# Performance work log

Hardware: AMD Instinct MI355X
Metric: run time of the kernel (lower is better)

The kernel has to match this reference:

```python
import jax, jax.numpy as jnp
import numpy as np
from jax import lax

# mamba-130m-style config
B, L = 2, 1024          # batch, seq_len
D = 768                 # hidden_size
E = 1536                # intermediate (expand=2)
N = 16                  # ssm state size
R = 48                  # time_step_rank = ceil(D/16)
K = 4                   # conv kernel
NL = 4                  # num layers
NC = 5                  # num classes
EPS = 1e-5


def setup_inputs() -> dict:
    key = jax.random.key(0)
    ks = jax.random.split(key, 10)
    s = 0.02
    return {
        "x": jax.random.normal(ks[0], (B, L, 12), dtype=jnp.float32),
        "proj_w": jax.random.normal(ks[1], (D, 12)) * s,
        "proj_b": jnp.zeros((D,), jnp.float32),
        "norm_w": jnp.ones((NL, D), jnp.float32),
        "in_w": jax.random.normal(ks[2], (NL, 2 * E, D)) * s,
        "conv_w": jax.random.normal(ks[3], (NL, E, K)) * s,
        "conv_b": jnp.zeros((NL, E), jnp.float32),
        "xproj_w": jax.random.normal(ks[4], (NL, R + 2 * N, E)) * s,
        "dt_w": jax.random.normal(ks[5], (NL, E, R)) * s,
        "dt_b": jnp.full((NL, E), -4.0, jnp.float32),  # softplus(-4) ~ small dt
        "A_log": jnp.tile(jnp.log(jnp.arange(1, N + 1, dtype=jnp.float32))[None, None, :], (NL, E, 1)),
        "D_param": jnp.ones((NL, E), jnp.float32),
        "out_w": jax.random.normal(ks[6], (NL, D, E)) * s,
        "fnorm_w": jnp.ones((D,), jnp.float32),
        "cls_w": jax.random.normal(ks[7], (NC, D)) * s,
        "cls_b": jnp.zeros((NC,), jnp.float32),
    }


def _rmsnorm(x, w):
    var = jnp.mean(x * x, axis=-1, keepdims=True)
    return x * lax.rsqrt(var + EPS) * w


def _causal_conv(u, w, b):
    # u: [B,L,E], w: [E,K] depthwise causal conv, left-pad K-1
    up = jnp.pad(u, ((0, 0), (K - 1, 0), (0, 0)))
    y = b
    for k in range(K):
        y = y + w[:, k] * up[:, k:k + L, :]
    return y


def _selective_scan(u, dt, A, Bm, Cm, Dp):
    # u, dt: [B,L,E]; Bm, Cm: [B,L,N]; A: [E,N]; Dp: [E]
    def step(h, inp):
        u_t, dt_t, B_t, C_t = inp  # [B,E],[B,E],[B,N],[B,N]
        dA = jnp.exp(dt_t[:, :, None] * A)                      # [B,E,N]
        h = h * dA + dt_t[:, :, None] * B_t[:, None, :] * u_t[:, :, None]
        y = jnp.einsum('ben,bn->be', h, C_t)
        return h, y

    h0 = jnp.zeros((u.shape[0], E, N), u.dtype)
    _, ys = lax.scan(step, h0,
                     (u.transpose(1, 0, 2), dt.transpose(1, 0, 2),
                      Bm.transpose(1, 0, 2), Cm.transpose(1, 0, 2)))
    return ys.transpose(1, 0, 2) + u * Dp


def reference(x, proj_w, proj_b, norm_w, in_w, conv_w, conv_b, xproj_w,
              dt_w, dt_b, A_log, D_param, out_w, fnorm_w, cls_w, cls_b):
    h = x @ proj_w.T + proj_b                                     # [B,L,D]
    for i in range(NL):
        res = h
        hn = _rmsnorm(h, norm_w[i])
        proj = hn @ in_w[i].T                                     # [B,L,2E]
        u, gate = proj[..., :E], proj[..., E:]
        u = jax.nn.silu(_causal_conv(u, conv_w[i], conv_b[i]))    # [B,L,E]
        xdbc = u @ xproj_w[i].T                                   # [B,L,R+2N]
        dt_r = xdbc[..., :R]
        Bm = xdbc[..., R:R + N]
        Cm = xdbc[..., R + N:]
        dt = jax.nn.softplus(dt_r @ dt_w[i].T + dt_b[i])          # [B,L,E]
        A = -jnp.exp(A_log[i])                                    # [E,N]
        y = _selective_scan(u, dt, A, Bm, Cm, D_param[i])
        y = y * jax.nn.silu(gate)
        h = res + y @ out_w[i].T
    h = _rmsnorm(h, fnorm_w)
    pooled = jnp.mean(h, axis=1)                                  # AdaptiveAvgPool1d(1)
    return pooled @ cls_w.T + cls_b                               # [B,NC]
```

## Files before the change

### kernel.cpp

```cpp
#include <hip/hip_runtime.h>

constexpr int B_  = 2;
constexpr int L_  = 1024;
constexpr int D_  = 768;
constexpr int E_  = 1536;
constexpr int N_  = 16;
constexpr int R_  = 48;
constexpr int NL_ = 4;
constexpr int NC_ = 5;
constexpr int M_  = B_ * L_;
constexpr int E2_ = 2 * E_;
constexpr int XD_ = R_ + 2 * N_;
constexpr float EPS_ = 1e-5f;

constexpr int NCH_ = 16;
constexpr int CL_  = L_ / NCH_;
constexpr int TS_  = 32;
constexpr int KS_  = 8;

typedef __attribute__((ext_vector_type(8))) short bf16x8;
typedef __attribute__((ext_vector_type(4))) float f32x4;
typedef const __attribute__((address_space(1))) void* gas_t;
typedef __attribute__((address_space(3))) void* las_t;

__device__ __forceinline__ float sigm(float x) { return 1.0f / (1.0f + __expf(-x)); }
__device__ __forceinline__ float softplusf(float x) { return x > 20.0f ? x : log1pf(__expf(x)); }
__device__ __forceinline__ ushort f2b(float f) {
  union { float f; unsigned u; } v; v.f = f;
  unsigned r = (v.u + 0x7fffu + ((v.u >> 16) & 1u)) >> 16;
  return (ushort)r;
}
__device__ __forceinline__ float b2f(ushort u) {
  union { unsigned u; float f; } v; v.u = ((unsigned)u) << 16;
  return v.f;
}

template <int CTRL>
__device__ __forceinline__ float dpp_add(float x) {
  int yi = __builtin_amdgcn_update_dpp(0, __builtin_bit_cast(int, x), CTRL, 0xf, 0xf, false);
  return x + __builtin_bit_cast(float, yi);
}
__device__ __forceinline__ float row_sum16(float x) {
  x = dpp_add<0x121>(x);
  x = dpp_add<0x122>(x);
  x = dpp_add<0x124>(x);
  x = dpp_add<0x128>(x);
  return x;
}

__device__ __forceinline__ float block_sum(float v, float* sm) {
  #pragma unroll
  for (int o = 32; o > 0; o >>= 1) v += __shfl_xor(v, o);
  if ((threadIdx.x & 63) == 0) sm[threadIdx.x >> 6] = v;
  __syncthreads();
  return sm[0] + sm[1] + sm[2] + sm[3];
}

__global__ __launch_bounds__(256) void k_f2b(const float* __restrict__ s, ushort* __restrict__ d, int nv) {
  int i = (blockIdx.x * 256 + threadIdx.x) * 4;
  if (i >= nv) return;
  float4 v = *(const float4*)(s + i);
  ushort4 o = make_ushort4(f2b(v.x), f2b(v.y), f2b(v.z), f2b(v.w));
  *(ushort4*)(d + i) = o;
}

__global__ __launch_bounds__(256) void k_dtpad(const float* __restrict__ dw, ushort* __restrict__ o) {
  int i = blockIdx.x * 256 + threadIdx.x;
  int k = i & 63, e = i >> 6;
  o[i] = (k < R_) ? f2b(dw[e * R_ + k]) : (ushort)0;
}

__global__ __launch_bounds__(256) void k_proj(const float* __restrict__ x, const float* __restrict__ pw,
                                              const float* __restrict__ pb, float* __restrict__ h) {
  __shared__ float xs[12];
  int m = blockIdx.y;
  int d = blockIdx.x * 256 + threadIdx.x;
  if (threadIdx.x < 12) xs[threadIdx.x] = x[m * 12 + threadIdx.x];
  __syncthreads();
  float acc = pb[d];
  #pragma unroll
  for (int j = 0; j < 12; j++) acc = fmaf(xs[j], pw[d * 12 + j], acc);
  h[(size_t)m * D_ + d] = acc;
}

__global__ __launch_bounds__(256) void k_rmsnorm_bf(const float* __restrict__ h, const float* __restrict__ w,
                                                    ushort* __restrict__ hn) {
  __shared__ float sm[4];
  int m = blockIdx.x, tid = threadIdx.x;
  const float* row = h + (size_t)m * D_;
  float v0 = row[tid], v1 = row[tid + 256], v2 = row[tid + 512];
  float s = block_sum(v0 * v0 + v1 * v1 + v2 * v2, sm);
  float sc = rsqrtf(s * (1.0f / D_) + EPS_);
  ushort* o = hn + (size_t)m * D_;
  o[tid]       = f2b(v0 * sc * w[tid]);
  o[tid + 256] = f2b(v1 * sc * w[tid + 256]);
  o[tid + 512] = f2b(v2 * sc * w[tid + 512]);
}

template <int BM, int BN, int MODE>
__global__ __launch_bounds__(256) void k_gemm_bf(const ushort* __restrict__ A, const ushort* __restrict__ Bw,
                                                 float* __restrict__ C, const float* __restrict__ res,
                                                 int Kd, int Nd) {
  constexpr int AM = BM / 32, BNF = BN / 32;
  __shared__ ushort sA[BM * 32];
  __shared__ ushort sB[BN * 32];
  const int tid = threadIdx.x;
  const int wave = tid >> 6, lane = tid & 63;
  const int q = lane >> 4, r = lane & 15;
  const int wm = wave >> 1, wn = wave & 1;
  const int m0 = blockIdx.y * BM, n0 = blockIdx.x * BN;
  f32x4 acc[AM][BNF] = {};

  for (int k0 = 0; k0 < Kd; k0 += 32) {
    #pragma unroll
    for (int j = 0; j < BM / 64; j++) {
      int i = j * 256 + tid;
      const ushort* gp = A + (size_t)(m0 + (i >> 2)) * Kd + k0 + ((i & 3) << 3);
      __builtin_amdgcn_global_load_lds((gas_t)gp, (las_t)(sA + ((j * 256 + wave * 64) << 3)), 16, 0, 0);
    }
    #pragma unroll
    for (int j = 0; j < BN / 64; j++) {
      int i = j * 256 + tid;
      const ushort* gp = Bw + (size_t)(n0 + (i >> 2)) * Kd + k0 + ((i & 3) << 3);
      __builtin_amdgcn_global_load_lds((gas_t)gp, (las_t)(sB + ((j * 256 + wave * 64) << 3)), 16, 0, 0);
    }
    __syncthreads();
    bf16x8 af[AM], bfv[BNF];
    #pragma unroll
    for (int mi = 0; mi < AM; mi++)
      af[mi] = *(const bf16x8*)&sA[(wm * (BM / 2) + mi * 16 + r) * 32 + q * 8];
    #pragma unroll
    for (int nj = 0; nj < BNF; nj++)
      bfv[nj] = *(const bf16x8*)&sB[(wn * (BN / 2) + nj * 16 + r) * 32 + q * 8];
    #pragma unroll
    for (int mi = 0; mi < AM; mi++)
      #pragma unroll
      for (int nj = 0; nj < BNF; nj++)
        acc[mi][nj] = __builtin_amdgcn_mfma_f32_16x16x32_bf16(af[mi], bfv[nj], acc[mi][nj], 0, 0, 0);
    __syncthreads();
  }
  #pragma unroll
  for (int mi = 0; mi < AM; mi++) {
    #pragma unroll
    for (int nj = 0; nj < BNF; nj++) {
      int col = n0 + wn * (BN / 2) + nj * 16 + r;
      #pragma unroll
      for (int rg = 0; rg < 4; rg++) {
        int row = m0 + wm * (BM / 2) + mi * 16 + q * 4 + rg;
        size_t off = (size_t)row * Nd + col;
        float v = acc[mi][nj][rg];
        if (MODE == 1) v += res[off];
        if (MODE == 2) v = softplusf(v + res[col]);
        C[off] = v;
      }
    }
  }
}

__global__ __launch_bounds__(256) void k_gemm_x(const ushort* __restrict__ A, const ushort* __restrict__ Bw,
                                                float* __restrict__ part) {
  __shared__ ushort sA[64 * 32];
  __shared__ ushort sB[80 * 32];
  const int tid = threadIdx.x;
  const int wave = tid >> 6, lane = tid & 63;
  const int q = lane >> 4, r = lane & 15;
  const int m0 = blockIdx.x * 64;
  const int kbeg = blockIdx.y * (E_ / KS_), kend = kbeg + E_ / KS_;
  f32x4 acc[5] = {};

  for (int k0 = kbeg; k0 < kend; k0 += 32) {
    {
      const ushort* gp = A + (size_t)(m0 + wave * 16 + (lane >> 2)) * E_ + k0 + ((lane & 3) << 3);
      __builtin_amdgcn_global_load_lds((gas_t)gp, (las_t)(sA + (wave << 9)), 16, 0, 0);
    }
    #pragma unroll
    for (int j = wave; j < 5; j += 4) {
      const ushort* gp = Bw + (size_t)(j * 16 + (lane >> 2)) * E_ + k0 + ((lane & 3) << 3);
      __builtin_amdgcn_global_load_lds((gas_t)gp, (las_t)(sB + (j << 9)), 16, 0, 0);
    }
    __syncthreads();
    bf16x8 af = *(const bf16x8*)&sA[(wave * 16 + r) * 32 + q * 8];
    #pragma unroll
    for (int nj = 0; nj < 5; nj++) {
      bf16x8 bfv = *(const bf16x8*)&sB[(nj * 16 + r) * 32 + q * 8];
      acc[nj] = __builtin_amdgcn_mfma_f32_16x16x32_bf16(af, bfv, acc[nj], 0, 0, 0);
    }
    __syncthreads();
  }
  float* pp = part + (size_t)blockIdx.y * M_ * XD_;
  #pragma unroll
  for (int nj = 0; nj < 5; nj++) {
    int col = nj * 16 + r;
    #pragma unroll
    for (int rg = 0; rg < 4; rg++) {
      int row = m0 + wave * 16 + q * 4 + rg;
      pp[(size_t)row * XD_ + col] = acc[nj][rg];
    }
  }
}

__global__ __launch_bounds__(256) void k_xfin(const float* __restrict__ part, float* __restrict__ xdbc,
                                              ushort* __restrict__ xb) {
  int i = blockIdx.x * 256 + threadIdx.x;
  int m = i / XD_, col = i - m * XD_;
  float s = 0.0f;
  #pragma unroll
  for (int ks = 0; ks < KS_; ks++) s += part[(size_t)ks * M_ * XD_ + i];
  xdbc[i] = s;
  if (col < R_) xb[(size_t)m * 64 + col] = f2b(s);
  else if (col < 64) xb[(size_t)m * 64 + col] = 0;
}

__global__ __launch_bounds__(256) void k_conv(const float* __restrict__ proj, const float* __restrict__ cw,
                                              const float* __restrict__ cb, ushort* __restrict__ ub16) {
  int m = blockIdx.y;
  int b = m >> 10, t = m & (L_ - 1);
  int e = blockIdx.x * 256 + threadIdx.x;
  float4 w = *(const float4*)(cw + e * 4);
  float wr[4] = {w.x, w.y, w.z, w.w};
  float acc = cb[e];
  #pragma unroll
  for (int k = 0; k < 4; k++) {
    int tt = t + k - 3;
    if (tt >= 0) acc = fmaf(wr[k], proj[(size_t)(b * L_ + tt) * E2_ + e], acc);
  }
  float uv = acc * sigm(acc);
  ub16[(size_t)m * E_ + e] = f2b(uv);
}


__global__ __launch_bounds__(256) void k_scanA(const ushort* __restrict__ u, const float* __restrict__ dtb,
                                               const float* __restrict__ xdbc, const float* __restrict__ A_log,
                                               float* __restrict__ Pst, float* __restrict__ Sst) {
  __shared__ float2 s_dtu[2][TS_][16];
  __shared__ float  s_b [2][TS_][16];
  const int tid = threadIdx.x;
  const int e0 = blockIdx.x << 4;
  const int b  = blockIdx.y;
  const int c  = blockIdx.z;
  const int n  = tid & 15, el = tid >> 4;
  const int e  = e0 + el;
  const float A = -__expf(A_log[e * N_ + n]);
  const int se = tid & 15, st = tid >> 4;

  float r_dt[2], r_b[2];
  ushort r_u[2];
  auto issue = [&](int s) {
    int t0 = c * CL_ + s * TS_;
    #pragma unroll
    for (int j = 0; j < 2; j++) {
      size_t m = (size_t)(b * L_ + t0 + j * 16 + st);
      r_dt[j] = dtb[m * E_ + e0 + se];
      r_u[j]  = u[m * E_ + e0 + se];
    }
    #pragma unroll
    for (int j = 0; j < 2; j++) {
      int idx = j * 256 + tid;
      r_b[j] = xdbc[(size_t)(b * L_ + t0 + (idx >> 4)) * XD_ + R_ + (idx & 15)];
    }
  };
  auto commit = [&](int pb) {
    #pragma unroll
    for (int j = 0; j < 2; j++) {
      int t = j * 16 + st;
      s_dtu[pb][t][se] = make_float2(r_dt[j], r_dt[j] * b2f(r_u[j]));
    }
    #pragma unroll
    for (int j = 0; j < 2; j++) {
      int idx = j * 256 + tid;
      s_b[pb][idx >> 4][idx & 15] = r_b[j];
    }
  };

  issue(0);
  commit(0);
  float hs = 0.0f, pp = 1.0f;
  constexpr int NS = CL_ / TS_;
  for (int s = 0; s < NS; s++) {
    __syncthreads();
    if (s + 1 < NS) issue(s + 1);
    const int pb = s & 1;
    #pragma unroll
    for (int t = 0; t < TS_; t++) {
      float2 dtu = s_dtu[pb][t][el];
      float bv   = s_b[pb][t][n];
      float dA = __expf(dtu.x * A);
      hs = fmaf(hs, dA, dtu.y * bv);
      pp *= dA;
    }
    if (s + 1 < NS) commit((s + 1) & 1);
  }
  size_t o = (((size_t)(b * NCH_ + c) * E_) + e) * N_ + n;
  Pst[o] = pp;
  Sst[o] = hs;
}

__global__ __launch_bounds__(256) void k_scanC(const ushort* __restrict__ u, const float* __restrict__ dtb,
                                               const float* __restrict__ xdbc, const float* __restrict__ proj,
                                               const float* __restrict__ A_log, const float* __restrict__ Dp,
                                               const float* __restrict__ Pst, const float* __restrict__ Sst,
                                               ushort* __restrict__ y) {
  __shared__ float2 s_dtu[2][TS_][16];
  __shared__ float2 s_bc [2][TS_][16];
  __shared__ float2 s_og [2][TS_][16];
  const int tid = threadIdx.x;
  const int e0 = blockIdx.x << 4;
  const int b  = blockIdx.y;
  const int c  = blockIdx.z;
  const int n  = tid & 15, el = tid >> 4;
  const int e  = e0 + el;
  const float A = -__expf(A_log[e * N_ + n]);
  const int se = tid & 15, st = tid >> 4;
  const float Dv = Dp[e0 + se];

  float r_dt[2], r_g[2], r_bc[4];
  ushort r_u[2];
  auto issue = [&](int s) {
    int t0 = c * CL_ + s * TS_;
    #pragma unroll
    for (int j = 0; j < 2; j++) {
      size_t m = (size_t)(b * L_ + t0 + j * 16 + st);
      r_dt[j] = dtb[m * E_ + e0 + se];
      r_u[j]  = u[m * E_ + e0 + se];
      r_g[j]  = proj[m * E2_ + E_ + e0 + se];
    }
    #pragma unroll
    for (int j = 0; j < 4; j++) {
      int idx = j * 256 + tid;
      r_bc[j] = xdbc[(size_t)(b * L_ + t0 + (idx >> 5)) * XD_ + R_ + (idx & 31)];
    }
  };
  auto commit = [&](int pb) {
    #pragma unroll
    for (int j = 0; j < 2; j++) {
      int t = j * 16 + st;
      float uf = b2f(r_u[j]);
      s_dtu[pb][t][se] = make_float2(r_dt[j], r_dt[j] * uf);
      float g = r_g[j];
      s_og[pb][t][se] = make_float2(uf * Dv, g * sigm(g));
    }
    #pragma unroll
    for (int j = 0; j < 4; j++) {
      int idx = j * 256 + tid;
      int t = idx >> 5, col = idx & 31;
      ((float*)&s_bc[pb][t][0])[((col & 15) << 1) + (col >> 4)] = r_bc[j];
    }
  };

  issue(0);
  float hs = 0.0f;
  for (int cc = 0; cc < c; cc++) {
    size_t o = (((size_t)(b * NCH_ + cc) * E_) + e) * N_ + n;
    hs = fmaf(Pst[o], hs, Sst[o]);
  }
  commit(0);
  constexpr int NS = CL_ / TS_;
  for (int s = 0; s < NS; s++) {
    __syncthreads();
    if (s + 1 < NS) issue(s + 1);
    const int pb = s & 1;
    const int mbase = b * L_ + c * CL_ + s * TS_;
    #pragma unroll
    for (int t = 0; t < TS_; t++) {
      float2 dtu = s_dtu[pb][t][el];
      float2 bc  = s_bc[pb][t][n];
      float dA = __expf(dtu.x * A);
      hs = fmaf(hs, dA, dtu.y * bc.x);
      float p = row_sum16(hs * bc.y);
      if (n == 0) {
        float2 og = s_og[pb][t][el];
        y[(size_t)(mbase + t) * E_ + e] = f2b((p + og.x) * og.y);
      }
    }
    if (s + 1 < NS) commit((s + 1) & 1);
  }
}

__global__ __launch_bounds__(256) void k_rowscale(const float* __restrict__ h, float* __restrict__ rs) {
  __shared__ float sm[4];
  int m = blockIdx.x, tid = threadIdx.x;
  const float* row = h + (size_t)m * D_;
  float v0 = row[tid], v1 = row[tid + 256], v2 = row[tid + 512];
  float s = block_sum(v0 * v0 + v1 * v1 + v2 * v2, sm);
  if (tid == 0) rs[m] = rsqrtf(s * (1.0f / D_) + EPS_);
}

__global__ __launch_bounds__(256) void k_pool(const float* __restrict__ h, const float* __restrict__ rs,
                                              const float* __restrict__ fw, float* __restrict__ pooled) {
  int d = blockIdx.x * 256 + threadIdx.x;
  int t0 = blockIdx.y * 128;
  int b = blockIdx.z;
  float acc = 0.0f;
  for (int t = t0; t < t0 + 128; t++) {
    int m = b * L_ + t;
    acc = fmaf(h[(size_t)m * D_ + d], rs[m], acc);
  }
  atomicAdd(&pooled[b * D_ + d], acc * fw[d] * (1.0f / L_));
}

__global__ __launch_bounds__(256) void k_logits(const float* __restrict__ pooled, const float* __restrict__ cw,
                                                const float* __restrict__ cb, float* __restrict__ out) {
  int wv = threadIdx.x >> 6, ln = threadIdx.x & 63;
  for (int p = wv; p < B_ * NC_; p += 4) {
    int b = p / NC_, c = p % NC_;
    float s = 0.0f;
    for (int d = ln; d < D_; d += 64) s = fmaf(pooled[b * D_ + d], cw[c * D_ + d], s);
    #pragma unroll
    for (int o = 32; o > 0; o >>= 1) s += __shfl_xor(s, o);
    if (ln == 0) out[p] = s + cb[c];
  }
}

extern "C" void kernel_launch(void* const* d_in, const int* in_sizes, int n_in,
                              void* d_out, int out_size, void* d_ws, size_t ws_size,
                              hipStream_t stream) {
  const float* x       = (const float*)d_in[0];
  const float* proj_w  = (const float*)d_in[1];
  const float* proj_b  = (const float*)d_in[2];
  const float* norm_w  = (const float*)d_in[3];
  const float* in_w    = (const float*)d_in[4];
  const float* conv_w  = (const float*)d_in[5];
  const float* conv_b  = (const float*)d_in[6];
  const float* xproj_w = (const float*)d_in[7];
  const float* dt_w    = (const float*)d_in[8];
  const float* dt_b    = (const float*)d_in[9];
  const float* A_log   = (const float*)d_in[10];
  const float* D_param = (const float*)d_in[11];
  const float* out_w   = (const float*)d_in[12];
  const float* fnorm_w = (const float*)d_in[13];
  const float* cls_w   = (const float*)d_in[14];
  const float* cls_b   = (const float*)d_in[15];
  float* out = (float*)d_out;

  float* h      = (float*)d_ws;
  float* proj   = h + (size_t)M_ * D_;
  float* xdbc   = proj + (size_t)M_ * E2_;
  float* dtbuf  = xdbc + (size_t)M_ * XD_;
  float* rsb    = dtbuf + (size_t)M_ * E_;
  float* pooled = rsb + M_;
  float* Pst    = pooled + B_ * D_;
  float* Sst    = Pst + (size_t)B_ * NCH_ * E_ * N_;
  float* xpart  = Sst + (size_t)B_ * NCH_ * E_ * N_;
  ushort* hn_bf   = (ushort*)(xpart + (size_t)KS_ * M_ * XD_);
  ushort* y_bf    = hn_bf + (size_t)M_ * D_;
  ushort* ub_bf   = y_bf + (size_t)M_ * E_;
  ushort* xdbc_bf = ub_bf + (size_t)M_ * E_;
  ushort* xwb     = xdbc_bf + (size_t)M_ * 64;
  ushort* dtwb    = xwb + (size_t)NL_ * XD_ * E_;
  ushort* in_wb   = dtwb + (size_t)NL_ * E_ * 64;
  ushort* out_wb  = in_wb + (size_t)NL_ * E2_ * D_;

  k_f2b<<<(NL_ * XD_ * E_ / 4 + 255) / 256, 256, 0, stream>>>(xproj_w, xwb, NL_ * XD_ * E_);
  k_dtpad<<<NL_ * E_ * 64 / 256, 256, 0, stream>>>(dt_w, dtwb);
  k_f2b<<<(NL_ * E2_ * D_ / 4 + 255) / 256, 256, 0, stream>>>(in_w, in_wb, NL_ * E2_ * D_);
  k_f2b<<<(NL_ * D_ * E_ / 4 + 255) / 256, 256, 0, stream>>>(out_w, out_wb, NL_ * D_ * E_);

  k_proj<<<dim3(D_ / 256, M_), 256, 0, stream>>>(x, proj_w, proj_b, h);

  for (int i = 0; i < NL_; i++) {
    k_rmsnorm_bf<<<M_, 256, 0, stream>>>(h, norm_w + i * D_, hn_bf);
    k_gemm_bf<128, 128, 0><<<dim3(E2_ / 128, M_ / 128), 256, 0, stream>>>(
        hn_bf, in_wb + (size_t)i * E2_ * D_, proj, nullptr, D_, E2_);
    k_conv<<<dim3(E_ / 256, M_), 256, 0, stream>>>(proj, conv_w + i * E_ * 4, conv_b + i * E_, ub_bf);
    k_gemm_x<<<dim3(M_ / 64, KS_), 256, 0, stream>>>(ub_bf, xwb + (size_t)i * XD_ * E_, xpart);
    k_xfin<<<M_ * XD_ / 256, 256, 0, stream>>>(xpart, xdbc, xdbc_bf);
    k_gemm_bf<64, 128, 2><<<dim3(E_ / 128, M_ / 64), 256, 0, stream>>>(
        xdbc_bf, dtwb + (size_t)i * E_ * 64, dtbuf, dt_b + i * E_, 64, E_);
    k_scanA<<<dim3(E_ / 16, B_, NCH_), 256, 0, stream>>>(ub_bf, dtbuf, xdbc,
                                                         A_log + (size_t)i * E_ * N_, Pst, Sst);
    k_scanC<<<dim3(E_ / 16, B_, NCH_), 256, 0, stream>>>(ub_bf, dtbuf, xdbc, proj,
                                                         A_log + (size_t)i * E_ * N_, D_param + i * E_,
                                                         Pst, Sst, y_bf);
    k_gemm_bf<64, 128, 1><<<dim3(D_ / 128, M_ / 64), 256, 0, stream>>>(
        y_bf, out_wb + (size_t)i * D_ * E_, h, h, E_, D_);
  }

  k_rowscale<<<M_, 256, 0, stream>>>(h, rsb);
  hipMemsetAsync(pooled, 0, (size_t)B_ * D_ * sizeof(float), stream);
  k_pool<<<dim3(D_ / 256, L_ / 128, B_), 256, 0, stream>>>(h, rsb, fnorm_w, pooled);
  k_logits<<<1, 256, 0, stream>>>(pooled, cls_w, cls_b, out);
}
```

Measured before the change: 736.0 us.

## Store in-projection in bf16, vectorize conv with gate silu, merge weight prep kernels

The in-projection GEMM now writes bf16 output instead of fp32, uses 64-row tiles, and a new vectorized conv kernel reads the bf16 projection to produce both the conv+SiLU activations and a precomputed SiLU gate in bf16, which the scan reads directly. The four weight-conversion launches are merged into one kernel, and the dt and out-projection GEMMs switch to 64x64 tiles for more blocks. The intent is to cut memory traffic on the large proj buffer, cut launch count, and raise occupancy on the smaller GEMMs. The cost is extra rounding of the projection and gate to bf16.

```diff
diff --git a/kernel.cpp b/kernel.cpp
--- a/kernel.cpp
+++ b/kernel.cpp
@@ -34,6 +34,14 @@
   union { unsigned u; float f; } v; v.u = ((unsigned)u) << 16;
   return v.f;
 }
+__device__ __forceinline__ float b2f_lo(unsigned p) {
+  union { unsigned u; float f; } v; v.u = p << 16;
+  return v.f;
+}
+__device__ __forceinline__ float b2f_hi(unsigned p) {
+  union { unsigned u; float f; } v; v.u = p & 0xffff0000u;
+  return v.f;
+}
 
 template <int CTRL>
 __device__ __forceinline__ float dpp_add(float x) {
@@ -56,18 +64,36 @@
   return sm[0] + sm[1] + sm[2] + sm[3];
 }
 
-__global__ __launch_bounds__(256) void k_f2b(const float* __restrict__ s, ushort* __restrict__ d, int nv) {
+constexpr int WS1_ = NL_ * E2_ * D_;
+constexpr int WS2_ = NL_ * D_ * E_;
+constexpr int WS3_ = NL_ * XD_ * E_;
+constexpr int WS4_ = NL_ * E_ * 64;
+__global__ __launch_bounds__(256) void k_wprep(const float* __restrict__ in_w, const float* __restrict__ out_w,
+                                               const float* __restrict__ xw, const float* __restrict__ dw,
+                                               ushort* __restrict__ in_wb, ushort* __restrict__ out_wb,
+                                               ushort* __restrict__ xwb, ushort* __restrict__ dtwb) {
   int i = (blockIdx.x * 256 + threadIdx.x) * 4;
-  if (i >= nv) return;
-  float4 v = *(const float4*)(s + i);
-  ushort4 o = make_ushort4(f2b(v.x), f2b(v.y), f2b(v.z), f2b(v.w));
-  *(ushort4*)(d + i) = o;
-}
-
-__global__ __launch_bounds__(256) void k_dtpad(const float* __restrict__ dw, ushort* __restrict__ o) {
-  int i = blockIdx.x * 256 + threadIdx.x;
-  int k = i & 63, e = i >> 6;
-  o[i] = (k < R_) ? f2b(dw[e * R_ + k]) : (ushort)0;
+  if (i < WS1_) {
+    float4 v = *(const float4*)(in_w + i);
+    *(ushort4*)(in_wb + i) = make_ushort4(f2b(v.x), f2b(v.y), f2b(v.z), f2b(v.w));
+  } else if (i < WS1_ + WS2_) {
+    int j = i - WS1_;
+    float4 v = *(const float4*)(out_w + j);
+    *(ushort4*)(out_wb + j) = make_ushort4(f2b(v.x), f2b(v.y), f2b(v.z), f2b(v.w));
+  } else if (i < WS1_ + WS2_ + WS3_) {
+    int j = i - WS1_ - WS2_;
+    float4 v = *(const float4*)(xw + j);
+    *(ushort4*)(xwb + j) = make_ushort4(f2b(v.x), f2b(v.y), f2b(v.z), f2b(v.w));
+  } else if (i < WS1_ + WS2_ + WS3_ + WS4_) {
+    int j = i - WS1_ - WS2_ - WS3_;
+    int k = j & 63, e = j >> 6;
+    ushort4 o;
+    o.x = (k + 0 < R_) ? f2b(dw[e * R_ + k + 0]) : (ushort)0;
+    o.y = (k + 1 < R_) ? f2b(dw[e * R_ + k + 1]) : (ushort)0;
+    o.z = (k + 2 < R_) ? f2b(dw[e * R_ + k + 2]) : (ushort)0;
+    o.w = (k + 3 < R_) ? f2b(dw[e * R_ + k + 3]) : (ushort)0;
+    *(ushort4*)(dtwb + j) = o;
+  }
 }
 
 __global__ __launch_bounds__(256) void k_proj(const float* __restrict__ x, const float* __restrict__ pw,
@@ -99,7 +125,7 @@
 
 template <int BM, int BN, int MODE>
 __global__ __launch_bounds__(256) void k_gemm_bf(const ushort* __restrict__ A, const ushort* __restrict__ Bw,
-                                                 float* __restrict__ C, const float* __restrict__ res,
+                                                 void* __restrict__ Cv, const float* __restrict__ res,
                                                  int Kd, int Nd) {
   constexpr int AM = BM / 32, BNF = BN / 32;
   __shared__ ushort sA[BM * 32];
@@ -149,9 +175,13 @@
         int row = m0 + wm * (BM / 2) + mi * 16 + q * 4 + rg;
         size_t off = (size_t)row * Nd + col;
         float v = acc[mi][nj][rg];
-        if (MODE == 1) v += res[off];
-        if (MODE == 2) v = softplusf(v + res[col]);
-        C[off] = v;
+        if (MODE == 3) {
+          ((ushort*)Cv)[off] = f2b(v);
+        } else {
+          if (MODE == 1) v += res[off];
+          if (MODE == 2) v = softplusf(v + res[col]);
+          ((float*)Cv)[off] = v;
+        }
       }
     }
   }
@@ -211,23 +241,47 @@
   else if (col < 64) xb[(size_t)m * 64 + col] = 0;
 }
 
-__global__ __launch_bounds__(256) void k_conv(const float* __restrict__ proj, const float* __restrict__ cw,
-                                              const float* __restrict__ cb, ushort* __restrict__ ub16) {
-  int m = blockIdx.y;
+__global__ __launch_bounds__(384) void k_conv2(const ushort* __restrict__ proj, const float* __restrict__ cw,
+                                               const float* __restrict__ cb, ushort* __restrict__ ub16,
+                                               ushort* __restrict__ gb16) {
+  int m = blockIdx.x;
   int b = m >> 10, t = m & (L_ - 1);
-  int e = blockIdx.x * 256 + threadIdx.x;
-  float4 w = *(const float4*)(cw + e * 4);
-  float wr[4] = {w.x, w.y, w.z, w.w};
-  float acc = cb[e];
+  int e4 = threadIdx.x * 4;
+  float wv[4][4];
+  #pragma unroll
+  for (int j = 0; j < 4; j++) {
+    float4 w = *(const float4*)(cw + (e4 + j) * 4);
+    wv[j][0] = w.x; wv[j][1] = w.y; wv[j][2] = w.z; wv[j][3] = w.w;
+  }
+  float4 bb = *(const float4*)(cb + e4);
+  float acc[4] = {bb.x, bb.y, bb.z, bb.w};
   #pragma unroll
   for (int k = 0; k < 4; k++) {
     int tt = t + k - 3;
-    if (tt >= 0) acc = fmaf(wr[k], proj[(size_t)(b * L_ + tt) * E2_ + e], acc);
-  }
-  float uv = acc * sigm(acc);
-  ub16[(size_t)m * E_ + e] = f2b(uv);
-}
-
+    if (tt >= 0) {
+      uint2 p = *(const uint2*)(proj + (size_t)(b * L_ + tt) * E2_ + e4);
+      acc[0] = fmaf(wv[0][k], b2f_lo(p.x), acc[0]);
+      acc[1] = fmaf(wv[1][k], b2f_hi(p.x), acc[1]);
+      acc[2] = fmaf(wv[2][k], b2f_lo(p.y), acc[2]);
+      acc[3] = fmaf(wv[3][k], b2f_hi(p.y), acc[3]);
+    }
+  }
+  uint2 uo;
+  {
+    float u0 = acc[0] * sigm(acc[0]), u1 = acc[1] * sigm(acc[1]);
+    float u2 = acc[2] * sigm(acc[2]), u3 = acc[3] * sigm(acc[3]);
+    uo.x = (unsigned)f2b(u0) | ((unsigned)f2b(u1) << 16);
+    uo.y = (unsigned)f2b(u2) | ((unsigned)f2b(u3) << 16);
+  }
+  *(uint2*)(ub16 + (size_t)m * E_ + e4) = uo;
+  uint2 g = *(const uint2*)(proj + (size_t)m * E2_ + E_ + e4);
+  float g0 = b2f_lo(g.x), g1 = b2f_hi(g.x), g2 = b2f_lo(g.y), g3 = b2f_hi(g.y);
+  g0 *= sigm(g0); g1 *= sigm(g1); g2 *= sigm(g2); g3 *= sigm(g3);
+  uint2 go;
+  go.x = (unsigned)f2b(g0) | ((unsigned)f2b(g1) << 16);
+  go.y = (unsigned)f2b(g2) | ((unsigned)f2b(g3) << 16);
+  *(uint2*)(gb16 + (size_t)m * E_ + e4) = go;
+}
 
 __global__ __launch_bounds__(256) void k_scanA(const ushort* __restrict__ u, const float* __restrict__ dtb,
                                                const float* __restrict__ xdbc, const float* __restrict__ A_log,
@@ -296,7 +350,7 @@
 }
 
 __global__ __launch_bounds__(256) void k_scanC(const ushort* __restrict__ u, const float* __restrict__ dtb,
-                                               const float* __restrict__ xdbc, const float* __restrict__ proj,
+                                               const float* __restrict__ xdbc, const ushort* __restrict__ gb,
                                                const float* __restrict__ A_log, const float* __restrict__ Dp,
                                                const float* __restrict__ Pst, const float* __restrict__ Sst,
                                                ushort* __restrict__ y) {
@@ -313,8 +367,8 @@
   const int se = tid & 15, st = tid >> 4;
   const float Dv = Dp[e0 + se];
 
-  float r_dt[2], r_g[2], r_bc[4];
-  ushort r_u[2];
+  float r_dt[2], r_bc[4];
+  ushort r_u[2], r_g[2];
   auto issue = [&](int s) {
     int t0 = c * CL_ + s * TS_;
     #pragma unroll
@@ -322,7 +376,7 @@
       size_t m = (size_t)(b * L_ + t0 + j * 16 + st);
       r_dt[j] = dtb[m * E_ + e0 + se];
       r_u[j]  = u[m * E_ + e0 + se];
-      r_g[j]  = proj[m * E2_ + E_ + e0 + se];
+      r_g[j]  = gb[m * E_ + e0 + se];
     }
     #pragma unroll
     for (int j = 0; j < 4; j++) {
@@ -336,8 +390,7 @@
       int t = j * 16 + st;
       float uf = b2f(r_u[j]);
       s_dtu[pb][t][se] = make_float2(r_dt[j], r_dt[j] * uf);
-      float g = r_g[j];
-      s_og[pb][t][se] = make_float2(uf * Dv, g * sigm(g));
+      s_og[pb][t][se] = make_float2(uf * Dv, b2f(r_g[j]));
     }
     #pragma unroll
     for (int j = 0; j < 4; j++) {
@@ -433,45 +486,45 @@
   float* out = (float*)d_out;
 
   float* h      = (float*)d_ws;
-  float* proj   = h + (size_t)M_ * D_;
-  float* xdbc   = proj + (size_t)M_ * E2_;
+  float* xdbc   = h + (size_t)M_ * D_;
   float* dtbuf  = xdbc + (size_t)M_ * XD_;
   float* rsb    = dtbuf + (size_t)M_ * E_;
   float* pooled = rsb + M_;
   float* Pst    = pooled + B_ * D_;
   float* Sst    = Pst + (size_t)B_ * NCH_ * E_ * N_;
   float* xpart  = Sst + (size_t)B_ * NCH_ * E_ * N_;
-  ushort* hn_bf   = (ushort*)(xpart + (size_t)KS_ * M_ * XD_);
+  ushort* proj_bf = (ushort*)(xpart + (size_t)KS_ * M_ * XD_);
+  ushort* hn_bf   = proj_bf + (size_t)M_ * E2_;
   ushort* y_bf    = hn_bf + (size_t)M_ * D_;
   ushort* ub_bf   = y_bf + (size_t)M_ * E_;
-  ushort* xdbc_bf = ub_bf + (size_t)M_ * E_;
+  ushort* g_bf    = ub_bf + (size_t)M_ * E_;
+  ushort* xdbc_bf = g_bf + (size_t)M_ * E_;
   ushort* xwb     = xdbc_bf + (size_t)M_ * 64;
   ushort* dtwb    = xwb + (size_t)NL_ * XD_ * E_;
   ushort* in_wb   = dtwb + (size_t)NL_ * E_ * 64;
   ushort* out_wb  = in_wb + (size_t)NL_ * E2_ * D_;
 
-  k_f2b<<<(NL_ * XD_ * E_ / 4 + 255) / 256, 256, 0, stream>>>(xproj_w, xwb, NL_ * XD_ * E_);
-  k_dtpad<<<NL_ * E_ * 64 / 256, 256, 0, stream>>>(dt_w, dtwb);
-  k_f2b<<<(NL_ * E2_ * D_ / 4 + 255) / 256, 256, 0, stream>>>(in_w, in_wb, NL_ * E2_ * D_);
-  k_f2b<<<(NL_ * D_ * E_ / 4 + 255) / 256, 256, 0, stream>>>(out_w, out_wb, NL_ * D_ * E_);
+  constexpr int WTOT = WS1_ + WS2_ + WS3_ + WS4_;
+  k_wprep<<<(WTOT / 4 + 255) / 256, 256, 0, stream>>>(in_w, out_w, xproj_w, dt_w,
+                                                      in_wb, out_wb, xwb, dtwb);
 
   k_proj<<<dim3(D_ / 256, M_), 256, 0, stream>>>(x, proj_w, proj_b, h);
 
   for (int i = 0; i < NL_; i++) {
     k_rmsnorm_bf<<<M_, 256, 0, stream>>>(h, norm_w + i * D_, hn_bf);
-    k_gemm_bf<128, 128, 0><<<dim3(E2_ / 128, M_ / 128), 256, 0, stream>>>(
-        hn_bf, in_wb + (size_t)i * E2_ * D_, proj, nullptr, D_, E2_);
-    k_conv<<<dim3(E_ / 256, M_), 256, 0, stream>>>(proj, conv_w + i * E_ * 4, conv_b + i * E_, ub_bf);
+    k_gemm_bf<64, 128, 3><<<dim3(E2_ / 128, M_ / 64), 256, 0, stream>>>(
+        hn_bf, in_wb + (size_t)i * E2_ * D_, proj_bf, nullptr, D_, E2_);
+    k_conv2<<<M_, 384, 0, stream>>>(proj_bf, conv_w + i * E_ * 4, conv_b + i * E_, ub_bf, g_bf);
     k_gemm_x<<<dim3(M_ / 64, KS_), 256, 0, stream>>>(ub_bf, xwb + (size_t)i * XD_ * E_, xpart);
     k_xfin<<<M_ * XD_ / 256, 256, 0, stream>>>(xpart, xdbc, xdbc_bf);
-    k_gemm_bf<64, 128, 2><<<dim3(E_ / 128, M_ / 64), 256, 0, stream>>>(
+    k_gemm_bf<64, 64, 2><<<dim3(E_ / 64, M_ / 64), 256, 0, stream>>>(
         xdbc_bf, dtwb + (size_t)i * E_ * 64, dtbuf, dt_b + i * E_, 64, E_);
     k_scanA<<<dim3(E_ / 16, B_, NCH_), 256, 0, stream>>>(ub_bf, dtbuf, xdbc,
                                                          A_log + (size_t)i * E_ * N_, Pst, Sst);
-    k_scanC<<<dim3(E_ / 16, B_, NCH_), 256, 0, stream>>>(ub_bf, dtbuf, xdbc, proj,
+    k_scanC<<<dim3(E_ / 16, B_, NCH_), 256, 0, stream>>>(ub_bf, dtbuf, xdbc, g_bf,
                                                          A_log + (size_t)i * E_ * N_, D_param + i * E_,
                                                          Pst, Sst, y_bf);
-    k_gemm_bf<64, 128, 1><<<dim3(D_ / 128, M_ / 64), 256, 0, stream>>>(
+    k_gemm_bf<64, 64, 1><<<dim3(D_ / 64, M_ / 64), 256, 0, stream>>>(
         y_bf, out_wb + (size_t)i * D_ * E_, h, h, E_, D_);
   }
 
```

After: 692.2 us. -5.9%, faster.
